# Kernel optimization log

Hardware: AMD Instinct MI355X
Metric: run time of the kernel (lower is better)

Reference implementation:

```python
import jax, jax.numpy as jnp
import numpy as np

B, E, T, H = 2, 1024, 2048, 16
DH = E // H


def _conv1x1(x, W, b, mask):
    # x: [B,C,T], W: [O,C], b: [O], mask: [B,1,T] (norm=False -> plain conv on masked input)
    x = x * mask
    return jnp.einsum('oc,bct->bot', W, x) + b[None, :, None]


def setup_inputs() -> dict:
    key = jax.random.key(0)
    ks = jax.random.split(key, 16)
    inp = {
        'q': jax.random.normal(ks[0], (B, E, T), jnp.float32),
        'k': jax.random.normal(ks[1], (B, E, T), jnp.float32),
        'v': jax.random.normal(ks[2], (B, E, T), jnp.float32),
        'query_mask': (jax.random.uniform(ks[3], (B, 1, T)) < 0.9).astype(jnp.float32),
        'key_mask': (jax.random.uniform(ks[4], (B, 1, T)) < 0.9).astype(jnp.float32),
        'value_mask': (jax.random.uniform(ks[5], (B, 1, T)) < 0.9).astype(jnp.float32),
        'Wq': jax.random.normal(ks[6], (E, E), jnp.float32) * (1.0 / np.sqrt(E)),
        'bq': jnp.zeros((E,), jnp.float32),
        'Wk': jax.random.normal(ks[7], (E, E), jnp.float32) * (1.0 / np.sqrt(E)),
        'bk': jnp.zeros((E,), jnp.float32),
        'Wv': jax.random.normal(ks[8], (E, E), jnp.float32) * (1.0 / np.sqrt(E)),
        'bv': jnp.zeros((E,), jnp.float32),
        'Wo': jax.random.normal(ks[9], (E, E), jnp.float32) * (1.0 / np.sqrt(E)),
        'bo': jnp.zeros((E,), jnp.float32),
    }
    return inp


def reference(q, k, v, query_mask, key_mask, value_mask, Wq, bq, Wk, bk, Wv, bv, Wo, bo):
    # 1x1 conv projections with input masking (norm=False path)
    qp = _conv1x1(q, Wq, bq, query_mask)   # [B,E,T]
    kp = _conv1x1(k, Wk, bk, key_mask)
    vp = _conv1x1(v, Wv, bv, value_mask)
    # split heads: [B,E,T] -> [B,H,DH,T]
    qh = qp.reshape(B, H, DH, T)
    kh = kp.reshape(B, H, DH, T)
    vh = vp.reshape(B, H, DH, T)
    # scores = q^T k with pre-softmax multiplicative masks, scaled by sqrt(embed_dim)
    scores = jnp.einsum('bhdq,bhdk->bhqk', qh, kh)
    scores = scores * query_mask[:, :, :, None] * key_mask[:, :, None, :] / np.sqrt(E)
    attn = jax.nn.softmax(scores, axis=-1) * key_mask[:, :, None, :]  # post-softmax mask
    # transpose_scores=False path: v @ scores (contracts v's time dim with the query dim)
    out = jnp.einsum('bhdq,bhqk->bhdk', vh, attn)  # [B,H,DH,T]
    out = out.reshape(B, E, T)
    return _conv1x1(out, Wo, bo, key_mask)
```

## Files before the change

### kernel.cpp

```cpp
#include <hip/hip_runtime.h>

#define B 2
#define E 1024
#define T 2048
#define H 16
#define DH 64

#define SCALE2 0.0450842200277801f

typedef _Float16 f16x8 __attribute__((ext_vector_type(8)));
typedef float f32x4 __attribute__((ext_vector_type(4)));
typedef float f32x16 __attribute__((ext_vector_type(16)));
typedef unsigned short ushort8v __attribute__((ext_vector_type(8)));
typedef unsigned int uint4v __attribute__((ext_vector_type(4)));

__device__ __forceinline__ f32x4 mfma16(f16x8 a, f16x8 b, f32x4 c) {
  return __builtin_amdgcn_mfma_f32_16x16x32_f16(a, b, c, 0, 0, 0);
}
__device__ __forceinline__ f32x16 mfma32(f16x8 a, f16x8 b, f32x16 c) {
  return __builtin_amdgcn_mfma_f32_32x32x16_f16(a, b, c, 0, 0, 0);
}
__device__ __forceinline__ unsigned short f16u(float x) {
  _Float16 h = (_Float16)x;
  return __builtin_bit_cast(unsigned short, h);
}
__device__ __forceinline__ float ex2(float x) {
  return __builtin_amdgcn_exp2f(x);
}
__device__ __forceinline__ unsigned int pk16(float a, float b) {
  auto h = __builtin_amdgcn_cvt_pkrtz(a, b);
  return __builtin_bit_cast(unsigned int, h);
}
__device__ __forceinline__ void plswap(unsigned int& a, unsigned int& b) {
  auto r = __builtin_amdgcn_permlane32_swap(a, b, false, false);
  a = r[0];
  b = r[1];
}

__global__ __launch_bounds__(256) void prep_weights(
    const float* __restrict__ Wq, const float* __restrict__ Wk,
    const float* __restrict__ Wv, const float* __restrict__ Wo,
    unsigned short* __restrict__ WqB, unsigned short* __restrict__ WkB,
    unsigned short* __restrict__ WvB, unsigned short* __restrict__ WoB) {
  const int which = blockIdx.y;
  const int i = (blockIdx.x * 256 + threadIdx.x) * 4;
  const float* src = which == 0 ? Wq : which == 1 ? Wk : which == 2 ? Wv : Wo;
  unsigned short* dst = which == 0 ? WqB : which == 1 ? WkB : which == 2 ? WvB : WoB;
  float4 v = *(const float4*)&src[i];
  ((unsigned int*)&dst[i])[0] = f16u(v.x) | ((unsigned)f16u(v.y) << 16);
  ((unsigned int*)&dst[i])[1] = f16u(v.z) | ((unsigned)f16u(v.w) << 16);
}

__global__ __launch_bounds__(256) void transpose_cvt(
    const float* __restrict__ q, const float* __restrict__ k,
    const float* __restrict__ v, unsigned short* __restrict__ XtQ,
    unsigned short* __restrict__ XtK, unsigned short* __restrict__ XtV) {
  __shared__ float Xs[32 * 36];
  const int z = blockIdx.z, which = z >> 1, b = z & 1;
  const float* X = which == 0 ? q : which == 1 ? k : v;
  unsigned short* O = which == 0 ? XtQ : which == 1 ? XtK : XtV;
  const int e0 = blockIdx.y * 32, t0 = blockIdx.x * 32;
  const int tid = threadIdx.x;
  const int r = tid >> 3, c = (tid & 7) * 4;
  *(float4*)&Xs[r * 36 + c] = *(const float4*)&X[((size_t)b * E + e0 + r) * T + t0 + c];
  __syncthreads();
  unsigned short h[4];
#pragma unroll
  for (int j = 0; j < 4; ++j) h[j] = f16u(Xs[(c + j) * 36 + r]);
  const size_t o = ((size_t)b * T + t0 + r) * E + e0 + c;
  ((unsigned int*)&O[o])[0] = h[0] | ((unsigned)h[1] << 16);
  ((unsigned int*)&O[o])[1] = h[2] | ((unsigned)h[3] << 16);
}

__global__ __launch_bounds__(256) void proj_qkv(
    const unsigned short* __restrict__ WqB, const unsigned short* __restrict__ WkB,
    const unsigned short* __restrict__ WvB, const unsigned short* __restrict__ XtQ,
    const unsigned short* __restrict__ XtK, const unsigned short* __restrict__ XtV,
    const float* __restrict__ bq, const float* __restrict__ bk,
    const float* __restrict__ bv, const float* __restrict__ qmask,
    const float* __restrict__ kmask, const float* __restrict__ vmask,
    unsigned short* __restrict__ qp2, unsigned short* __restrict__ kp2,
    unsigned short* __restrict__ vp) {
  __shared__ unsigned short Ah[128 * 72], Bs[128 * 72];
  const int b = blockIdx.z, my = blockIdx.y;
  const int which = my >> 3, o0 = (my & 7) * 128, t0 = blockIdx.x * 128;
  const unsigned short* W = which == 0 ? WqB : which == 1 ? WkB : WvB;
  const unsigned short* Xt = which == 0 ? XtQ : which == 1 ? XtK : XtV;
  const float* bias = which == 0 ? bq : which == 1 ? bk : bv;
  const float* mask = which == 0 ? qmask : which == 1 ? kmask : vmask;

  const int tid = threadIdx.x, wave = tid >> 6, lane = tid & 63;
  const int lg = lane & 15, quad = lane >> 4;
  const int wm = (wave & 1) * 64, wn = (wave >> 1) * 64;
  const int sr = tid >> 3, sc = (tid & 7) * 8;

  f32x4 acc[4][4];
#pragma unroll
  for (int i = 0; i < 4; ++i)
#pragma unroll
    for (int j = 0; j < 4; ++j) acc[i][j] = (f32x4){0.f, 0.f, 0.f, 0.f};

  for (int k0 = 0; k0 < E; k0 += 64) {
    ushort8v ra[4], rb[4];
#pragma unroll
    for (int p = 0; p < 4; ++p) {
      ra[p] = *(const ushort8v*)&W[(size_t)(o0 + p * 32 + sr) * E + k0 + sc];
      rb[p] = *(const ushort8v*)&Xt[((size_t)b * T + t0 + p * 32 + sr) * E + k0 + sc];
    }
    __syncthreads();
#pragma unroll
    for (int p = 0; p < 4; ++p) {
      *(ushort8v*)&Ah[(p * 32 + sr) * 72 + sc] = ra[p];
      *(ushort8v*)&Bs[(p * 32 + sr) * 72 + sc] = rb[p];
    }
    __syncthreads();
    f16x8 af[4][2];
#pragma unroll
    for (int mt = 0; mt < 4; ++mt) {
      af[mt][0] = *(const f16x8*)&Ah[(wm + mt * 16 + lg) * 72 + quad * 8];
      af[mt][1] = *(const f16x8*)&Ah[(wm + mt * 16 + lg) * 72 + 32 + quad * 8];
    }
#pragma unroll
    for (int nt = 0; nt < 4; ++nt) {
      f16x8 b0 = *(const f16x8*)&Bs[(wn + nt * 16 + lg) * 72 + quad * 8];
      f16x8 b1 = *(const f16x8*)&Bs[(wn + nt * 16 + lg) * 72 + 32 + quad * 8];
#pragma unroll
      for (int mt = 0; mt < 4; ++mt) {
        f32x4 c = acc[mt][nt];
        c = mfma16(af[mt][0], b0, c);
        c = mfma16(af[mt][1], b1, c);
        acc[mt][nt] = c;
      }
    }
  }
#pragma unroll
  for (int nt = 0; nt < 4; ++nt) {
    const int tcol = t0 + wn + nt * 16 + lg;
    const float mv = mask[b * T + tcol];
#pragma unroll
    for (int mt = 0; mt < 4; ++mt) {
      const int oF = o0 + wm + mt * 16 + quad * 4;
      float v4[4];
      if (which == 0) {
        const float s = mv * SCALE2;
#pragma unroll
        for (int r = 0; r < 4; ++r) v4[r] = (acc[mt][nt][r] + bias[oF + r]) * s;
      } else if (which == 1) {
#pragma unroll
        for (int r = 0; r < 4; ++r) v4[r] = (acc[mt][nt][r] + bias[oF + r]) * mv;
      } else {
#pragma unroll
        for (int r = 0; r < 4; ++r) v4[r] = acc[mt][nt][r] * mv + bias[oF + r];
      }
      if (which <= 1) {
        unsigned short* O = which == 0 ? qp2 : kp2;
        const int head = (o0 + wm) >> 6;
        const int bh2 = b * H + head;
        const size_t idx8 =
            (((size_t)(bh2 * (T / 32) + (tcol >> 5)) * 4 + mt) * 32 + (tcol & 31)) * 2 +
            (quad >> 1);
        unsigned int* dst = (unsigned int*)(O + idx8 * 8 + (quad & 1) * 4);
        dst[0] = f16u(v4[0]) | ((unsigned)f16u(v4[1]) << 16);
        dst[1] = f16u(v4[2]) | ((unsigned)f16u(v4[3]) << 16);
      } else {
#pragma unroll
        for (int r = 0; r < 4; ++r)
          vp[((size_t)b * E + oF + r) * T + tcol] = f16u(v4[r]);
      }
    }
  }
}

__global__ __launch_bounds__(256) void repack_v(
    const unsigned short* __restrict__ vp, unsigned short* __restrict__ vp2) {
  __shared__ unsigned short Ls[64 * 136];
  const int q0 = blockIdx.x * 128, hh = blockIdx.y, b = blockIdx.z;
  const int bh = b * H + hh;
  const int tid = threadIdx.x;
#pragma unroll
  for (int w = 0; w < 2; ++w) {
    const int d = w * 32 + (tid >> 3);
    const int c = (tid & 7) * 16;
    const unsigned short* src = vp + ((size_t)b * E + hh * DH + d) * T + q0 + c;
    *(ushort8v*)&Ls[d * 136 + c] = *(const ushort8v*)src;
    *(ushort8v*)&Ls[d * 136 + c + 8] = *(const ushort8v*)(src + 8);
  }
  __syncthreads();
#pragma unroll
  for (int w = 0; w < 4; ++w) {
    const int flat = w * 256 + tid;
    const int hb = flat & 1, lnv = (flat >> 1) & 31, dt = (flat >> 6) & 1,
              qgl = flat >> 7;
    ushort8v val = *(const ushort8v*)&Ls[(dt * 32 + lnv) * 136 + qgl * 16 + hb * 8];
    const size_t idx8 =
        (((size_t)(bh * (T / 16) + (q0 >> 4) + qgl) * 2 + dt) * 32 + lnv) * 2 + hb;
    *(ushort8v*)&vp2[idx8 * 8] = val;
  }
}

__global__ __launch_bounds__(256) void attn_stats(
    const unsigned short* __restrict__ qp2, const unsigned short* __restrict__ kp2,
    float* __restrict__ sPart) {
  const int bh = blockIdx.y;
  const int z = blockIdx.z;
  const int q0 = blockIdx.x * 256;
  const int tid = threadIdx.x, wave = tid >> 6, lane = tid & 63;
  const int ln = lane & 31, half = lane >> 5;

  const int t32q = (q0 >> 5) + wave * 2;
  f16x8 aq[2][4];
#pragma unroll
  for (int qs = 0; qs < 2; ++qs)
#pragma unroll
    for (int s = 0; s < 4; ++s)
      aq[qs][s] = *(const f16x8*)&qp2[((((size_t)bh * (T / 32) + t32q + qs) * 4 + s) * 64 +
                                       ln * 2 + half) * 8];

  float lacc[32];
#pragma unroll
  for (int r = 0; r < 32; ++r) lacc[r] = 0.f;

  const int kbase = z * (T / 2);
  const int kend = kbase + T / 2;

  f16x8 bkr[2][4];
#pragma unroll
  for (int nt = 0; nt < 2; ++nt)
#pragma unroll
    for (int s = 0; s < 4; ++s)
      bkr[nt][s] = *(const f16x8*)&kp2[((((size_t)bh * (T / 32) + (kbase >> 5) + nt) * 4 +
                                         s) * 64 + ln * 2 + half) * 8];

  for (int kt = kbase; kt < kend; kt += 64) {
    const int kn = (kt + 64 < kend) ? kt + 64 : kbase;
    f16x8 nb[2][4];
#pragma unroll
    for (int nt = 0; nt < 2; ++nt)
#pragma unroll
      for (int s = 0; s < 4; ++s)
        nb[nt][s] =
            *(const f16x8*)&kp2[((((size_t)bh * (T / 32) + (kn >> 5) + nt) * 4 + s) * 64 +
                                 ln * 2 + half) * 8];
#pragma unroll
    for (int qs = 0; qs < 2; ++qs) {
      f32x16 S0 = {}, S1 = {};
#pragma unroll
      for (int s = 0; s < 4; ++s) {
        S0 = mfma32(aq[qs][s], bkr[0][s], S0);
        S1 = mfma32(aq[qs][s], bkr[1][s], S1);
      }
#pragma unroll
      for (int r = 0; r < 16; ++r) lacc[qs * 16 + r] += ex2(S0[r]) + ex2(S1[r]);
    }
#pragma unroll
    for (int nt = 0; nt < 2; ++nt)
#pragma unroll
      for (int s = 0; s < 4; ++s) bkr[nt][s] = nb[nt][s];
  }
#pragma unroll
  for (int off = 1; off < 32; off <<= 1)
#pragma unroll
    for (int r = 0; r < 32; ++r) lacc[r] += __shfl_xor(lacc[r], off, 64);
  if (ln == 0) {
#pragma unroll
    for (int qs = 0; qs < 2; ++qs)
#pragma unroll
      for (int t = 0; t < 4; ++t) {
        f32x4 o;
#pragma unroll
        for (int j = 0; j < 4; ++j) o[j] = lacc[qs * 16 + t * 4 + j];
        *(f32x4*)&sPart[((size_t)z * (B * H) + bh) * T + q0 + wave * 64 + qs * 32 +
                        t * 8 + half * 4] = o;
      }
  }
}

__global__ __launch_bounds__(256) void stats_merge(
    const float* __restrict__ sPart, float* __restrict__ lLog) {
  const int i = (blockIdx.x * 256 + threadIdx.x) * 4;
  const int N = B * H * T;
  f32x4 a = *(const f32x4*)&sPart[i];
  f32x4 b = *(const f32x4*)&sPart[N + i];
  f32x4 o;
#pragma unroll
  for (int j = 0; j < 4; ++j) o[j] = -__builtin_amdgcn_logf(a[j] + b[j]);
  *(f32x4*)&lLog[i] = o;
}

__global__ __launch_bounds__(256) void attn_apply(
    const unsigned short* __restrict__ qp2, const unsigned short* __restrict__ kp2,
    const unsigned short* __restrict__ vp2, const float* __restrict__ lLog,
    unsigned short* __restrict__ ao) {
  __shared__ float st[64 * 130];
  const int bh = blockIdx.y, b = bh >> 4, h = bh & 15;
  const int kblk = blockIdx.x * 128;
  const int tid = threadIdx.x, wave = tid >> 6, lane = tid & 63;
  const int ln = lane & 31, half = lane >> 5;
  const int kt = wave & 1, qh = wave >> 1;

  const int t32k = (kblk >> 5) + kt * 2;
  f16x8 bkk[2][4];
#pragma unroll
  for (int sub = 0; sub < 2; ++sub)
#pragma unroll
    for (int s = 0; s < 4; ++s)
      bkk[sub][s] = *(const f16x8*)&kp2[((((size_t)bh * (T / 32) + t32k + sub) * 4 + s) *
                                             64 + ln * 2 + half) * 8];

  f32x16 acc00 = {}, acc01 = {}, acc10 = {}, acc11 = {};
  const int qstart = qh * (T / 2);
  const int qend = qstart + T / 2;

  f16x8 aqN[4], avN[2][2];
#pragma unroll
  for (int s = 0; s < 4; ++s)
    aqN[s] = *(const f16x8*)&qp2[((((size_t)bh * (T / 32) + (qstart >> 5)) * 4 + s) * 64 +
                                  ln * 2 + half) * 8];
#pragma unroll
  for (int dt = 0; dt < 2; ++dt)
#pragma unroll
    for (int f = 0; f < 2; ++f)
      avN[dt][f] = *(const f16x8*)&vp2[((((size_t)bh * (T / 16) + (qstart >> 4) + f) * 2 +
                                         dt) * 32 + ln) * 16 + half * 8];

  for (int qt = qstart; qt < qend; qt += 32) {
    f16x8 aq[4], av[2][2];
#pragma unroll
    for (int s = 0; s < 4; ++s) aq[s] = aqN[s];
#pragma unroll
    for (int dt = 0; dt < 2; ++dt)
#pragma unroll
      for (int f = 0; f < 2; ++f) av[dt][f] = avN[dt][f];
    const int qn = qt + 32 < qend ? qt + 32 : qstart;
#pragma unroll
    for (int s = 0; s < 4; ++s)
      aqN[s] = *(const f16x8*)&qp2[((((size_t)bh * (T / 32) + (qn >> 5)) * 4 + s) * 64 +
                                    ln * 2 + half) * 8];
#pragma unroll
    for (int dt = 0; dt < 2; ++dt)
#pragma unroll
      for (int f = 0; f < 2; ++f)
        avN[dt][f] = *(const f16x8*)&vp2[((((size_t)bh * (T / 16) + (qn >> 4) + f) * 2 +
                                           dt) * 32 + ln) * 16 + half * 8];
    f32x4 ll[4];
#pragma unroll
    for (int t = 0; t < 4; ++t)
      ll[t] = *(const f32x4*)&lLog[(size_t)bh * T + qt + t * 8 + half * 4];
    f32x16 S0 = {}, S1 = {};
#pragma unroll
    for (int s = 0; s < 4; ++s) S0 = mfma32(aq[s], bkk[0][s], S0);
#pragma unroll
    for (int s = 0; s < 4; ++s) S1 = mfma32(aq[s], bkk[1][s], S1);
    {
      unsigned int w[8];
#pragma unroll
      for (int p = 0; p < 8; ++p) {
        const float e0 = ex2(S0[p * 2 + 0] + ll[p >> 1][(p & 1) * 2 + 0]);
        const float e1 = ex2(S0[p * 2 + 1] + ll[p >> 1][(p & 1) * 2 + 1]);
        w[p] = pk16(e0, e1);
      }
      plswap(w[0], w[2]);
      plswap(w[1], w[3]);
      plswap(w[4], w[6]);
      plswap(w[5], w[7]);
      uint4v f0v, f1v;
      f0v[0] = w[0]; f0v[1] = w[1]; f0v[2] = w[2]; f0v[3] = w[3];
      f1v[0] = w[4]; f1v[1] = w[5]; f1v[2] = w[6]; f1v[3] = w[7];
      const f16x8 pf0 = __builtin_bit_cast(f16x8, f0v);
      const f16x8 pf1 = __builtin_bit_cast(f16x8, f1v);
      acc00 = mfma32(av[0][0], pf0, acc00);
      acc00 = mfma32(av[0][1], pf1, acc00);
      acc01 = mfma32(av[1][0], pf0, acc01);
      acc01 = mfma32(av[1][1], pf1, acc01);
    }
    {
      unsigned int w[8];
#pragma unroll
      for (int p = 0; p < 8; ++p) {
        const float e0 = ex2(S1[p * 2 + 0] + ll[p >> 1][(p & 1) * 2 + 0]);
        const float e1 = ex2(S1[p * 2 + 1] + ll[p >> 1][(p & 1) * 2 + 1]);
        w[p] = pk16(e0, e1);
      }
      plswap(w[0], w[2]);
      plswap(w[1], w[3]);
      plswap(w[4], w[6]);
      plswap(w[5], w[7]);
      uint4v f0v, f1v;
      f0v[0] = w[0]; f0v[1] = w[1]; f0v[2] = w[2]; f0v[3] = w[3];
      f1v[0] = w[4]; f1v[1] = w[5]; f1v[2] = w[6]; f1v[3] = w[7];
      const f16x8 pf0 = __builtin_bit_cast(f16x8, f0v);
      const f16x8 pf1 = __builtin_bit_cast(f16x8, f1v);
      acc10 = mfma32(av[0][0], pf0, acc10);
      acc10 = mfma32(av[0][1], pf1, acc10);
      acc11 = mfma32(av[1][0], pf0, acc11);
      acc11 = mfma32(av[1][1], pf1, acc11);
    }
  }

  __syncthreads();
  if (qh == 1) {
#pragma unroll
    for (int i = 0; i < 16; ++i) {
      st[(0 * 16 + i) * 130 + kt * 65 + lane] = acc00[i];
      st[(1 * 16 + i) * 130 + kt * 65 + lane] = acc01[i];
      st[(2 * 16 + i) * 130 + kt * 65 + lane] = acc10[i];
      st[(3 * 16 + i) * 130 + kt * 65 + lane] = acc11[i];
    }
  }
  __syncthreads();
  if (qh == 0) {
#pragma unroll
    for (int i = 0; i < 16; ++i) {
      acc00[i] += st[(0 * 16 + i) * 130 + kt * 65 + lane];
      acc01[i] += st[(1 * 16 + i) * 130 + kt * 65 + lane];
      acc10[i] += st[(2 * 16 + i) * 130 + kt * 65 + lane];
      acc11[i] += st[(3 * 16 + i) * 130 + kt * 65 + lane];
    }
#pragma unroll
    for (int sub = 0; sub < 2; ++sub) {
      const int kcol = kblk + kt * 64 + sub * 32 + ln;
      const size_t obase = ((size_t)b * T + kcol) * E + h * DH;
#pragma unroll
      for (int dt = 0; dt < 2; ++dt) {
        const float* a = sub == 0 ? (dt ? (const float*)&acc01 : (const float*)&acc00)
                                  : (dt ? (const float*)&acc11 : (const float*)&acc10);
#pragma unroll
        for (int t = 0; t < 4; ++t) {
          uint2 wv;
          wv.x = f16u(a[t * 4 + 0]) | ((unsigned)f16u(a[t * 4 + 1]) << 16);
          wv.y = f16u(a[t * 4 + 2]) | ((unsigned)f16u(a[t * 4 + 3]) << 16);
          *(uint2*)&ao[obase + dt * 32 + t * 8 + half * 4] = wv;
        }
      }
    }
  }
}

__global__ __launch_bounds__(256) void proj_final(
    const unsigned short* __restrict__ WoB, const unsigned short* __restrict__ ao,
    const float* __restrict__ bo, const float* __restrict__ kmask,
    float* __restrict__ out) {
  __shared__ unsigned short As[64 * 68], Bs[128 * 68];
  const int b = blockIdx.z, o0 = blockIdx.y * 64, t0 = blockIdx.x * 128;
  const int tid = threadIdx.x, wave = tid >> 6, lane = tid & 63;
  const int ln = lane & 31, half = lane >> 5;
  const int wn = wave * 32;
  const int ar = tid >> 2, ac = (tid & 3) * 16;
  const int br = tid >> 1, bc = (tid & 1) * 32;

  f32x16 acc0 = {}, acc1 = {};

  for (int k0 = 0; k0 < E; k0 += 64) {
    ushort8v a0 = *(const ushort8v*)&WoB[(size_t)(o0 + ar) * E + k0 + ac];
    ushort8v a1 = *(const ushort8v*)&WoB[(size_t)(o0 + ar) * E + k0 + ac + 8];
    ushort8v b0 = *(const ushort8v*)&ao[((size_t)b * T + t0 + br) * E + k0 + bc];
    ushort8v b1 = *(const ushort8v*)&ao[((size_t)b * T + t0 + br) * E + k0 + bc + 8];
    ushort8v b2 = *(const ushort8v*)&ao[((size_t)b * T + t0 + br) * E + k0 + bc + 16];
    ushort8v b3 = *(const ushort8v*)&ao[((size_t)b * T + t0 + br) * E + k0 + bc + 24];
    __syncthreads();
    *(ushort8v*)&As[ar * 68 + ac] = a0;
    *(ushort8v*)&As[ar * 68 + ac + 8] = a1;
    *(ushort8v*)&Bs[br * 68 + bc] = b0;
    *(ushort8v*)&Bs[br * 68 + bc + 8] = b1;
    *(ushort8v*)&Bs[br * 68 + bc + 16] = b2;
    *(ushort8v*)&Bs[br * 68 + bc + 24] = b3;
    __syncthreads();
#pragma unroll
    for (int s = 0; s < 4; ++s) {
      f16x8 af0 = *(const f16x8*)&As[ln * 68 + s * 16 + half * 8];
      f16x8 af1 = *(const f16x8*)&As[(32 + ln) * 68 + s * 16 + half * 8];
      f16x8 bf = *(const f16x8*)&Bs[(wn + ln) * 68 + s * 16 + half * 8];
      acc0 = mfma32(af0, bf, acc0);
      acc1 = mfma32(af1, bf, acc1);
    }
  }
  const int tcol = t0 + wn + ln;
  const float mv = kmask[b * T + tcol];
#pragma unroll
  for (int dt = 0; dt < 2; ++dt) {
    const float* a = dt ? (const float*)&acc1 : (const float*)&acc0;
#pragma unroll
    for (int t = 0; t < 4; ++t)
#pragma unroll
      for (int j = 0; j < 4; ++j) {
        const int e = o0 + dt * 32 + t * 8 + half * 4 + j;
        out[((size_t)b * E + e) * T + tcol] = a[t * 4 + j] * mv + bo[e];
      }
  }
}

extern "C" void kernel_launch(void* const* d_in, const int* in_sizes, int n_in,
                              void* d_out, int out_size, void* d_ws, size_t ws_size,
                              hipStream_t stream) {
  const float* q = (const float*)d_in[0];
  const float* k = (const float*)d_in[1];
  const float* v = (const float*)d_in[2];
  const float* qmask = (const float*)d_in[3];
  const float* kmask = (const float*)d_in[4];
  const float* vmask = (const float*)d_in[5];
  const float* Wq = (const float*)d_in[6];
  const float* bq = (const float*)d_in[7];
  const float* Wk = (const float*)d_in[8];
  const float* bk = (const float*)d_in[9];
  const float* Wv = (const float*)d_in[10];
  const float* bv = (const float*)d_in[11];
  const float* Wo = (const float*)d_in[12];
  const float* bo = (const float*)d_in[13];

  char* w = (char*)d_ws;
  const size_t WB = (size_t)E * E * sizeof(unsigned short);
  const size_t TB = (size_t)B * T * E * sizeof(unsigned short);
  unsigned short* WqB = (unsigned short*)(w + 0 * WB);
  unsigned short* WkB = (unsigned short*)(w + 1 * WB);
  unsigned short* WvB = (unsigned short*)(w + 2 * WB);
  unsigned short* WoB = (unsigned short*)(w + 3 * WB);
  size_t off = 4 * WB;
  unsigned short* XtQ = (unsigned short*)(w + off); off += TB;
  unsigned short* qp2 = (unsigned short*)(w + off); off += TB;
  unsigned short* kp2 = (unsigned short*)(w + off); off += TB;
  unsigned short* vp2 = (unsigned short*)(w + off); off += TB;
  float* lLog = (float*)(w + off); off += (size_t)B * H * T * sizeof(float);
  float* sPart = (float*)(w + off); off += (size_t)2 * B * H * T * sizeof(float);
  unsigned short* XtK = (unsigned short*)(w + off); off += TB;
  unsigned short* XtV = (unsigned short*)(w + off); off += TB;
  unsigned short* vp  = (unsigned short*)(w + off); off += TB;
  unsigned short* ao = XtQ;

  dim3 bl(256);
  prep_weights<<<dim3((E * E) / 1024, 4), bl, 0, stream>>>(
      Wq, Wk, Wv, Wo, WqB, WkB, WvB, WoB);
  transpose_cvt<<<dim3(T / 32, E / 32, 3 * B), bl, 0, stream>>>(
      q, k, v, XtQ, XtK, XtV);
  proj_qkv<<<dim3(T / 128, 24, B), bl, 0, stream>>>(
      WqB, WkB, WvB, XtQ, XtK, XtV, bq, bk, bv, qmask, kmask, vmask, qp2, kp2, vp);
  repack_v<<<dim3(T / 128, H, B), bl, 0, stream>>>(vp, vp2);
  attn_stats<<<dim3(T / 256, B * H, 2), bl, 0, stream>>>(qp2, kp2, sPart);
  stats_merge<<<dim3((B * H * T) / 1024), bl, 0, stream>>>(sPart, lLog);
  attn_apply<<<dim3(T / 128, B * H), bl, 0, stream>>>(qp2, kp2, vp2, lLog, ao);
  proj_final<<<dim3(T / 128, E / 64, B), bl, 0, stream>>>(
      WoB, ao, bo, kmask, (float*)d_out);
}
```

Measured before the change: 276.8 us.

## Split attention apply over query halves with fp32 partials and a merge kernel

attn_apply now splits each block's query range into two grid slices, doubling the block count, and remaps block indices so heads interleave across the grid. Each slice writes fp32 partial outputs, and a new apply_merge kernel sums them and writes the f16 [B,T,E] layout. The log-normaliser is preloaded into the MFMA accumulator, which removes the per-element adds before exp2. The extra parallelism aims to improve occupancy and load balance, at the cost of an extra launch and a large fp32 partial buffer written and read back. That buffer aliases the XtK region and may extend past it.

Measured after the change: 291.0 us. +5.1%, slower.

```diff
diff --git a/kernel.cpp b/kernel.cpp
--- a/kernel.cpp
+++ b/kernel.cpp
@@ -290,10 +290,13 @@
 __global__ __launch_bounds__(256) void attn_apply(
     const unsigned short* __restrict__ qp2, const unsigned short* __restrict__ kp2,
     const unsigned short* __restrict__ vp2, const float* __restrict__ lLog,
-    unsigned short* __restrict__ ao) {
+    float* __restrict__ aPart) {
   __shared__ float st[64 * 130];
-  const int bh = blockIdx.y, b = bh >> 4, h = bh & 15;
-  const int kblk = blockIdx.x * 128;
+  const int n = blockIdx.x;
+  const int z = blockIdx.y;
+  const int s_ = n >> 3;
+  const int bh = (n & 7) * 4 + (s_ >> 4);
+  const int kblk = (s_ & 15) * 128;
   const int tid = threadIdx.x, wave = tid >> 6, lane = tid & 63;
   const int ln = lane & 31, half = lane >> 5;
   const int kt = wave & 1, qh = wave >> 1;
@@ -308,8 +311,8 @@
                                              64 + ln * 2 + half) * 8];
 
   f32x16 acc00 = {}, acc01 = {}, acc10 = {}, acc11 = {};
-  const int qstart = qh * (T / 2);
-  const int qend = qstart + T / 2;
+  const int qstart = (z * 2 + qh) * (T / 4);
+  const int qend = qstart + T / 4;
 
   f16x8 aqN[4], avN[2][2];
 #pragma unroll
@@ -346,7 +349,13 @@
 #pragma unroll
     for (int t = 0; t < 4; ++t)
       ll[t] = *(const f32x4*)&lLog[(size_t)bh * T + qt + t * 8 + half * 4];
-    f32x16 S0 = {}, S1 = {};
+    f32x16 S0, S1;
+#pragma unroll
+    for (int r = 0; r < 16; ++r) {
+      const float c = ll[r >> 2][r & 3];
+      S0[r] = c;
+      S1[r] = c;
+    }
 #pragma unroll
     for (int s = 0; s < 4; ++s) S0 = mfma32(aq[s], bkk[0][s], S0);
 #pragma unroll
@@ -354,11 +363,8 @@
     {
       unsigned int w[8];
 #pragma unroll
-      for (int p = 0; p < 8; ++p) {
-        const float e0 = ex2(S0[p * 2 + 0] + ll[p >> 1][(p & 1) * 2 + 0]);
-        const float e1 = ex2(S0[p * 2 + 1] + ll[p >> 1][(p & 1) * 2 + 1]);
-        w[p] = pk16(e0, e1);
-      }
+      for (int p = 0; p < 8; ++p)
+        w[p] = pk16(ex2(S0[p * 2 + 0]), ex2(S0[p * 2 + 1]));
       plswap(w[0], w[2]);
       plswap(w[1], w[3]);
       plswap(w[4], w[6]);
@@ -376,11 +382,8 @@
     {
       unsigned int w[8];
 #pragma unroll
-      for (int p = 0; p < 8; ++p) {
-        const float e0 = ex2(S1[p * 2 + 0] + ll[p >> 1][(p & 1) * 2 + 0]);
-        const float e1 = ex2(S1[p * 2 + 1] + ll[p >> 1][(p & 1) * 2 + 1]);
-        w[p] = pk16(e0, e1);
-      }
+      for (int p = 0; p < 8; ++p)
+        w[p] = pk16(ex2(S1[p * 2 + 0]), ex2(S1[p * 2 + 1]));
       plswap(w[0], w[2]);
       plswap(w[1], w[3]);
       plswap(w[4], w[6]);
@@ -419,21 +422,45 @@
 #pragma unroll
     for (int sub = 0; sub < 2; ++sub) {
       const int kcol = kblk + kt * 64 + sub * 32 + ln;
-      const size_t obase = ((size_t)b * T + kcol) * E + h * DH;
+      float* dst = aPart + ((size_t)(z * B * H + bh) * T + kcol) * DH;
 #pragma unroll
       for (int dt = 0; dt < 2; ++dt) {
         const float* a = sub == 0 ? (dt ? (const float*)&acc01 : (const float*)&acc00)
                                   : (dt ? (const float*)&acc11 : (const float*)&acc10);
 #pragma unroll
         for (int t = 0; t < 4; ++t) {
-          uint2 wv;
-          wv.x = f16u(a[t * 4 + 0]) | ((unsigned)f16u(a[t * 4 + 1]) << 16);
-          wv.y = f16u(a[t * 4 + 2]) | ((unsigned)f16u(a[t * 4 + 3]) << 16);
-          *(uint2*)&ao[obase + dt * 32 + t * 8 + half * 4] = wv;
+          f32x4 o;
+#pragma unroll
+          for (int j = 0; j < 4; ++j) o[j] = a[t * 4 + j];
+          *(f32x4*)&dst[dt * 32 + t * 8 + half * 4] = o;
         }
       }
     }
   }
+}
+
+__global__ __launch_bounds__(256) void apply_merge(
+    const float* __restrict__ aPart, unsigned short* __restrict__ ao) {
+  const size_t i = ((size_t)blockIdx.x * 256 + threadIdx.x) * 8;
+  const size_t NZ = (size_t)B * H * T * DH;
+  f32x4 a0 = *(const f32x4*)&aPart[i];
+  f32x4 a1 = *(const f32x4*)&aPart[i + 4];
+  f32x4 b0 = *(const f32x4*)&aPart[NZ + i];
+  f32x4 b1 = *(const f32x4*)&aPart[NZ + i + 4];
+  unsigned short h[8];
+#pragma unroll
+  for (int j = 0; j < 4; ++j) h[j] = f16u(a0[j] + b0[j]);
+#pragma unroll
+  for (int j = 0; j < 4; ++j) h[4 + j] = f16u(a1[j] + b1[j]);
+  const int bh = (int)(i >> 17);
+  const int rem = (int)(i & (T * DH - 1));
+  const int k = rem >> 6, d = rem & 63;
+  uint4v u;
+  u[0] = h[0] | ((unsigned)h[1] << 16);
+  u[1] = h[2] | ((unsigned)h[3] << 16);
+  u[2] = h[4] | ((unsigned)h[5] << 16);
+  u[3] = h[6] | ((unsigned)h[7] << 16);
+  *(uint4v*)&ao[((size_t)(bh >> 4) * T + k) * E + (bh & 15) * 64 + d] = u;
 }
 
 __global__ __launch_bounds__(256) void proj_final(
@@ -524,6 +551,7 @@
   unsigned short* XtK = (unsigned short*)(w + off); off += TB;
   unsigned short* XtV = (unsigned short*)(w + off); off += TB;
   unsigned short* vp  = (unsigned short*)(w + off); off += TB;
+  float* aPart = (float*)XtK;
   unsigned short* ao = XtQ;
 
   dim3 bl(256);
@@ -536,7 +564,8 @@
   repack_v<<<dim3(T / 128, H, B), bl, 0, stream>>>(vp, vp2);
   attn_stats<<<dim3(T / 256, B * H, 2), bl, 0, stream>>>(qp2, kp2, sPart);
   stats_merge<<<dim3((B * H * T) / 1024), bl, 0, stream>>>(sPart, lLog);
-  attn_apply<<<dim3(T / 128, B * H), bl, 0, stream>>>(qp2, kp2, vp2, lLog, ao);
+  attn_apply<<<dim3(512, 2), bl, 0, stream>>>(qp2, kp2, vp2, lLog, aPart);
+  apply_merge<<<dim3((B * H * T * DH) / 2048), bl, 0, stream>>>(aPart, ao);
   proj_final<<<dim3(T / 128, E / 64, B), bl, 0, stream>>>(
       WoB, ao, bo, kmask, (float*)d_out);
 }
```
